# Kernel tuning notes

Hardware: AMD Instinct MI355X
Metric: run time of the kernel (lower is better)

Reference implementation:

```python
import jax, jax.numpy as jnp
import numpy as np

L, D, F, H, E, V = 16, 256, 512, 8, 12, 52000  # layers, width, FFWidth, heads, experts, vocab
B, S = 4, 512
HD = D // H
EPS = 1e-5


def _ln(x, s, b):
    m = x.mean(-1, keepdims=True)
    v = ((x - m) ** 2).mean(-1, keepdims=True)
    return (x - m) / jnp.sqrt(v + EPS) * s + b


def setup_inputs() -> dict:
    key = jax.random.key(0)
    ks = jax.random.split(key, 12)
    w = lambda k, shape: (jax.random.normal(k, shape, dtype=jnp.float32) * 0.02)
    return {
        "tokens": jax.random.randint(ks[0], (B, S), 0, V),
        "emb": w(ks[1], (V, D)),
        "Wq": w(ks[2], (L, D, D)), "bq": jnp.zeros((L, D), jnp.float32),
        "Wk": w(ks[3], (L, D, D)), "bk": jnp.zeros((L, D), jnp.float32),
        "Wv": w(ks[4], (L, D, D)), "bv": jnp.zeros((L, D), jnp.float32),
        "ln1_s": jnp.ones((L, D), jnp.float32), "ln1_b": jnp.zeros((L, D), jnp.float32),
        "ln2_s": jnp.ones((L, D), jnp.float32), "ln2_b": jnp.zeros((L, D), jnp.float32),
        "gW": w(ks[5], (L, D, E)), "gb": jnp.zeros((L, E), jnp.float32),
        "ff1W": w(ks[6], (L, E, D, F)), "ff1b": jnp.zeros((L, E, F), jnp.float32),
        "ffGW": w(ks[7], (L, E, D, F)), "ffGb": jnp.zeros((L, E, F), jnp.float32),
        "ff2W": w(ks[8], (L, E, F, D)), "ff2b": jnp.zeros((L, E, D), jnp.float32),
    }


def _forward(tokens, emb, Wq, bq, Wk, bk, Wv, bv, ln1_s, ln1_b, ln2_s, ln2_b,
             gW, gb, ff1W, ff1b, ffGW, ffGb, ff2W, ff2b):
    x = emb[tokens]  # [B,S,D]
    causal = jnp.triu(jnp.full((S, S), -jnp.inf, dtype=x.dtype), 1)

    def body(x, p):
        (wq, bq_, wk, bk_, wv, bv_, l1s, l1b, l2s, l2b,
         gw, gb_, f1w, f1b, fgw, fgb, f2w, f2b) = p
        q = (x @ wq + bq_).reshape(B, S, H, HD)
        k = (x @ wk + bk_).reshape(B, S, H, HD)
        v = (x @ wv + bv_).reshape(B, S, H, HD)
        # NOTE: original applies no 1/sqrt(d) scaling -- kept faithful
        att = jnp.einsum('bshw,bShw->bhsS', q, k) + causal
        att = jax.nn.softmax(att, axis=-1)
        o = jnp.einsum('bhsS,bShw->bshw', att, v).reshape(B, S, D)
        norm = _ln(o + x, l1s, l1b)
        # MoE: top-2 experts, outputs SUMMED (no gate weighting, per original)
        probs = jax.nn.softmax(norm @ gw + gb_, axis=-1)
        _, idx = jax.lax.top_k(probs, 2)  # [B,S,2]
        msk = jax.nn.one_hot(idx, E, dtype=norm.dtype).sum(-2)  # [B,S,E] in {0,1}
        h = jax.nn.silu(jnp.einsum('bsd,edf->bsef', norm, f1w) + f1b) \
            * (jnp.einsum('bsd,edf->bsef', norm, fgw) + fgb)
        y = jnp.einsum('bsef,efd->bsed', h, f2w) + f2b
        moe = jnp.einsum('bsed,bse->bsd', y, msk)
        return _ln(moe + norm, l2s, l2b), None

    x, _ = jax.lax.scan(body, x, (Wq, bq, Wk, bk, Wv, bv, ln1_s, ln1_b, ln2_s, ln2_b,
                                  gW, gb, ff1W, ff1b, ffGW, ffGb, ff2W, ff2b))
    return x


def reference(tokens, emb, Wq, bq, Wk, bk, Wv, bv, ln1_s, ln1_b, ln2_s, ln2_b,
              gW, gb, ff1W, ff1b, ffGW, ffGb, ff2W, ff2b):
    return _forward(tokens, emb, Wq, bq, Wk, bk, Wv, bv, ln1_s, ln1_b, ln2_s, ln2_b,
                    gW, gb, ff1W, ff1b, ffGW, ffGb, ff2W, ff2b)
```

## Files before the change

### kernel.cpp

```cpp
#include <hip/hip_runtime.h>
#include <math.h>

#define LNUM 16
#define D 256
#define FF 512
#define NH 8
#define NE 12
#define HD 32
#define BB 4
#define SS 512
#define NT 2048
#define EPS 1e-5f
#define MAXT 48
#define PADROWS 5632

typedef _Float16 f16;
typedef __attribute__((ext_vector_type(8))) _Float16 f16x8;
typedef __attribute__((ext_vector_type(4))) _Float16 f16x4;
typedef __attribute__((ext_vector_type(4))) float f32x4;
#define MFMA(A, B, C) __builtin_amdgcn_mfma_f32_16x16x32_f16((A), (B), (C), 0, 0, 0)

__device__ inline void splitf(float x, f16& h, f16& l) {
  f16 hh = (f16)x;
  h = hh;
  l = (f16)(x - (float)hh);
}

__global__ __launch_bounds__(256) void k_wprep(const float* __restrict__ src,
                                               f16* __restrict__ dh, f16* __restrict__ dl,
                                               int K, int N) {
  const size_t msz = (size_t)K * N * blockIdx.z;
  src += msz; dh += msz; dl += msz;
  const int n0 = blockIdx.x * 32, k0 = blockIdx.y * 32;
  __shared__ f16 th[32][36], tl[32][36];
  const int t = threadIdx.x;
  {
    const int r = t >> 3, c4 = (t & 7) * 4;
    float4 v = *(const float4*)(src + (size_t)(k0 + r) * N + n0 + c4);
    f16 h0, l0, h1, l1, h2, l2, h3, l3;
    splitf(v.x, h0, l0); splitf(v.y, h1, l1);
    splitf(v.z, h2, l2); splitf(v.w, h3, l3);
    th[c4 + 0][r] = h0; tl[c4 + 0][r] = l0;
    th[c4 + 1][r] = h1; tl[c4 + 1][r] = l1;
    th[c4 + 2][r] = h2; tl[c4 + 2][r] = l2;
    th[c4 + 3][r] = h3; tl[c4 + 3][r] = l3;
  }
  __syncthreads();
  const int rn = t >> 3, ck = (t & 7) * 4;
  f16x4 hv, lv;
#pragma unroll
  for (int j = 0; j < 4; j++) { hv[j] = th[rn][ck + j]; lv[j] = tl[rn][ck + j]; }
  *(f16x4*)(dh + (size_t)(n0 + rn) * K + k0 + ck) = hv;
  *(f16x4*)(dl + (size_t)(n0 + rn) * K + k0 + ck) = lv;
}

__global__ __launch_bounds__(256) void k_embed(const int* __restrict__ tok,
                                               const float* __restrict__ emb,
                                               float* __restrict__ x,
                                               f16* __restrict__ xh, f16* __restrict__ xl) {
  int n = blockIdx.x, t = threadIdx.x;
  float val = emb[(size_t)tok[n] * D + t];
  x[(size_t)n * D + t] = val;
  f16 h, l; splitf(val, h, l);
  xh[(size_t)n * D + t] = h;
  xl[(size_t)n * D + t] = l;
}

__global__ __launch_bounds__(256) void k_qkv_mfma(
    const f16* __restrict__ xh, const f16* __restrict__ xl,
    const f16* __restrict__ wqh, const f16* __restrict__ wql, const float* __restrict__ bq,
    const f16* __restrict__ wkh, const f16* __restrict__ wkl, const float* __restrict__ bk,
    const f16* __restrict__ wvh, const f16* __restrict__ wvl, const float* __restrict__ bv,
    f16* __restrict__ qhb, f16* __restrict__ qlb,
    f16* __restrict__ khb, f16* __restrict__ klb,
    f16* __restrict__ vhb, f16* __restrict__ vlb) {
  const f16* Wh; const f16* Wl; const float* bias; f16* outh; f16* outl;
  if (blockIdx.z == 0)      { Wh = wqh; Wl = wql; bias = bq; outh = qhb; outl = qlb; }
  else if (blockIdx.z == 1) { Wh = wkh; Wl = wkl; bias = bk; outh = khb; outl = klb; }
  else                      { Wh = wvh; Wl = wvl; bias = bv; outh = vhb; outl = vlb; }
  const int row0 = blockIdx.x * 128, col0 = blockIdx.y * 64;
  __shared__ f16 Ah[128][44], Al[128][44], Bh[64][44], Bl[64][44];
  const int tid = threadIdx.x;
  const int asr = tid >> 1, asc = (tid & 1) * 16;
  const int bn2 = tid >> 2, bkc = (tid & 3) * 8;
  const int lane = tid & 63, w = tid >> 6;
  const int lm = lane & 15, lg = lane >> 4, lk = lg * 8;
  f32x4 acc[2][4] = {};
  for (int k0 = 0; k0 < D; k0 += 32) {
    {
      size_t ga = (size_t)(row0 + asr) * D + k0 + asc;
      *(f16x8*)&Ah[asr][asc]     = *(const f16x8*)(xh + ga);
      *(f16x8*)&Ah[asr][asc + 8] = *(const f16x8*)(xh + ga + 8);
      *(f16x8*)&Al[asr][asc]     = *(const f16x8*)(xl + ga);
      *(f16x8*)&Al[asr][asc + 8] = *(const f16x8*)(xl + ga + 8);
      size_t gb = (size_t)(col0 + bn2) * D + k0 + bkc;
      *(f16x8*)&Bh[bn2][bkc] = *(const f16x8*)(Wh + gb);
      *(f16x8*)&Bl[bn2][bkc] = *(const f16x8*)(Wl + gb);
    }
    __syncthreads();
    f16x8 a_h[2], a_l[2];
#pragma unroll
    for (int mt = 0; mt < 2; mt++) {
      a_h[mt] = *(const f16x8*)&Ah[w * 32 + mt * 16 + lm][lk];
      a_l[mt] = *(const f16x8*)&Al[w * 32 + mt * 16 + lm][lk];
    }
#pragma unroll
    for (int nt = 0; nt < 4; nt++) {
      f16x8 b_h = *(const f16x8*)&Bh[nt * 16 + lm][lk];
      f16x8 b_l = *(const f16x8*)&Bl[nt * 16 + lm][lk];
#pragma unroll
      for (int mt = 0; mt < 2; mt++) {
        f32x4 c = acc[mt][nt];
        c = MFMA(a_h[mt], b_h, c);
        c = MFMA(a_h[mt], b_l, c);
        c = MFMA(a_l[mt], b_h, c);
        acc[mt][nt] = c;
      }
    }
    __syncthreads();
  }
#pragma unroll
  for (int mt = 0; mt < 2; mt++)
#pragma unroll
    for (int nt = 0; nt < 4; nt++) {
      int col = col0 + nt * 16 + lm;
      float bv_ = bias[col];
#pragma unroll
      for (int r = 0; r < 4; r++) {
        int row = row0 + w * 32 + mt * 16 + lg * 4 + r;
        float val = acc[mt][nt][r] + bv_;
        f16 h16, l16; splitf(val, h16, l16);
        outh[(size_t)row * D + col] = h16;
        outl[(size_t)row * D + col] = l16;
      }
    }
}

__global__ __launch_bounds__(256) void k_attn_mfma(
    const f16* __restrict__ qh, const f16* __restrict__ ql,
    const f16* __restrict__ kh, const f16* __restrict__ kl,
    const f16* __restrict__ vh, const f16* __restrict__ vl,
    float* __restrict__ o) {
  const int rt = blockIdx.x, bh = blockIdx.y;
  const int b = bh >> 3, h = bh & 7;
  const int row0 = rt * 64;
  __shared__ f16 Qh[64][40], Ql[64][40], Kh[64][40], Kl[64][40];
  __shared__ f16 Vth[32][72], Vtl[32][72];
  __shared__ f16 Ph[4][16][72], Pl[4][16][72];
  const int tid = threadIdx.x;
  const int lane = tid & 63, w = tid >> 6;
  const int lm = lane & 15, lg = lane >> 4, lk = lg * 8;
  const int sr = tid >> 2, sc = (tid & 3) * 8;
  {
    size_t gq = (size_t)(b * SS + row0 + sr) * D + h * HD + sc;
    *(f16x8*)&Qh[sr][sc] = *(const f16x8*)(qh + gq);
    *(f16x8*)&Ql[sr][sc] = *(const f16x8*)(ql + gq);
  }
  f32x4 accO[2] = {};
  float mrow[4], lsum[4];
#pragma unroll
  for (int r = 0; r < 4; r++) { mrow[r] = -1e30f; lsum[r] = 0.f; }
  for (int ct = 0; ct <= rt; ct++) {
    __syncthreads();
    {
      size_t gk = (size_t)(b * SS + ct * 64 + sr) * D + h * HD + sc;
      *(f16x8*)&Kh[sr][sc] = *(const f16x8*)(kh + gk);
      *(f16x8*)&Kl[sr][sc] = *(const f16x8*)(kl + gk);
      f16x8 hv = *(const f16x8*)(vh + gk);
      f16x8 lv = *(const f16x8*)(vl + gk);
#pragma unroll
      for (int j = 0; j < 8; j++) { Vth[sc + j][sr] = hv[j]; Vtl[sc + j][sr] = lv[j]; }
    }
    __syncthreads();
    f16x8 qfh = *(const f16x8*)&Qh[w * 16 + lm][lk];
    f16x8 qfl = *(const f16x8*)&Ql[w * 16 + lm][lk];
    f32x4 s[4];
#pragma unroll
    for (int nt = 0; nt < 4; nt++) {
      f16x8 kfh = *(const f16x8*)&Kh[nt * 16 + lm][lk];
      f16x8 kfl = *(const f16x8*)&Kl[nt * 16 + lm][lk];
      f32x4 c = {};
      c = MFMA(qfh, kfh, c);
      c = MFMA(qfh, kfl, c);
      c = MFMA(qfl, kfh, c);
      s[nt] = c;
    }
    if (ct == rt) {
#pragma unroll
      for (int nt = 0; nt < 4; nt++)
#pragma unroll
        for (int r = 0; r < 4; r++)
          if (nt * 16 + lm > w * 16 + lg * 4 + r) s[nt][r] = -1e30f;
    }
    float scal[4];
#pragma unroll
    for (int r = 0; r < 4; r++) {
      float mt2 = fmaxf(fmaxf(s[0][r], s[1][r]), fmaxf(s[2][r], s[3][r]));
      mt2 = fmaxf(mt2, __shfl_xor(mt2, 1));
      mt2 = fmaxf(mt2, __shfl_xor(mt2, 2));
      mt2 = fmaxf(mt2, __shfl_xor(mt2, 4));
      mt2 = fmaxf(mt2, __shfl_xor(mt2, 8));
      float mn = fmaxf(mrow[r], mt2);
      scal[r] = expf(mrow[r] - mn);
      mrow[r] = mn;
    }
    float rs[4] = {0.f, 0.f, 0.f, 0.f};
#pragma unroll
    for (int nt = 0; nt < 4; nt++)
#pragma unroll
      for (int r = 0; r < 4; r++) {
        float pv = expf(s[nt][r] - mrow[r]);
        rs[r] += pv;
        f16 ph16, pl16; splitf(pv, ph16, pl16);
        Ph[w][lg * 4 + r][nt * 16 + lm] = ph16;
        Pl[w][lg * 4 + r][nt * 16 + lm] = pl16;
      }
#pragma unroll
    for (int r = 0; r < 4; r++) {
      rs[r] += __shfl_xor(rs[r], 1);
      rs[r] += __shfl_xor(rs[r], 2);
      rs[r] += __shfl_xor(rs[r], 4);
      rs[r] += __shfl_xor(rs[r], 8);
      lsum[r] = lsum[r] * scal[r] + rs[r];
      accO[0][r] *= scal[r];
      accO[1][r] *= scal[r];
    }
#pragma unroll
    for (int ct2 = 0; ct2 < 2; ct2++)
#pragma unroll
      for (int ks = 0; ks < 2; ks++) {
        f16x8 pa_h = *(const f16x8*)&Ph[w][lm][ks * 32 + lk];
        f16x8 pa_l = *(const f16x8*)&Pl[w][lm][ks * 32 + lk];
        f16x8 vb_h = *(const f16x8*)&Vth[ct2 * 16 + lm][ks * 32 + lk];
        f16x8 vb_l = *(const f16x8*)&Vtl[ct2 * 16 + lm][ks * 32 + lk];
        accO[ct2] = MFMA(pa_h, vb_h, accO[ct2]);
        accO[ct2] = MFMA(pa_h, vb_l, accO[ct2]);
        accO[ct2] = MFMA(pa_l, vb_h, accO[ct2]);
      }
  }
#pragma unroll
  for (int ct2 = 0; ct2 < 2; ct2++)
#pragma unroll
    for (int r = 0; r < 4; r++) {
      int grow = row0 + w * 16 + lg * 4 + r;
      o[(size_t)(b * SS + grow) * D + h * HD + ct2 * 16 + lm] = accO[ct2][r] / lsum[r];
    }
}

__global__ __launch_bounds__(256) void k_ln1gate(
    const float* __restrict__ o, const float* __restrict__ x,
    const float* __restrict__ s1, const float* __restrict__ b1,
    const float* __restrict__ gW, const float* __restrict__ gb,
    float* __restrict__ norm, f16* __restrict__ nhb, f16* __restrict__ nlb,
    int* __restrict__ eidx) {
  const int w = threadIdx.x >> 6, lane = threadIdx.x & 63;
  const int n = blockIdx.x * 4 + w;
  float val[4], s1v = 0.f, s2v = 0.f;
#pragma unroll
  for (int j = 0; j < 4; j++) {
    int d = lane + 64 * j;
    float v = o[(size_t)n * D + d] + x[(size_t)n * D + d];
    val[j] = v; s1v += v; s2v += v * v;
  }
#pragma unroll
  for (int m = 1; m < 64; m <<= 1) {
    s1v += __shfl_xor(s1v, m);
    s2v += __shfl_xor(s2v, m);
  }
  float mean = s1v * (1.f / D);
  float var = s2v * (1.f / D) - mean * mean;
  float rstd = rsqrtf(var + EPS);
  float ge[NE];
#pragma unroll
  for (int e = 0; e < NE; e++) ge[e] = 0.f;
#pragma unroll
  for (int j = 0; j < 4; j++) {
    int d = lane + 64 * j;
    float nv = (val[j] - mean) * rstd * s1[d] + b1[d];
    norm[(size_t)n * D + d] = nv;
    f16 h16, l16; splitf(nv, h16, l16);
    nhb[(size_t)n * D + d] = h16;
    nlb[(size_t)n * D + d] = l16;
    const float* gr = gW + (size_t)d * NE;
#pragma unroll
    for (int e = 0; e < NE; e++) ge[e] += nv * gr[e];
  }
#pragma unroll
  for (int m = 1; m < 64; m <<= 1)
#pragma unroll
    for (int e = 0; e < NE; e++) ge[e] += __shfl_xor(ge[e], m);
  if (lane == 0) {
#pragma unroll
    for (int e = 0; e < NE; e++) ge[e] += gb[e];
    int i1 = 0; float v1 = ge[0];
#pragma unroll
    for (int e = 1; e < NE; e++) if (ge[e] > v1) { v1 = ge[e]; i1 = e; }
    int i2 = -1; float v2 = -3.4e38f;
#pragma unroll
    for (int e = 0; e < NE; e++) if (e != i1 && ge[e] > v2) { v2 = ge[e]; i2 = e; }
    eidx[n * 2 + 0] = i1;
    eidx[n * 2 + 1] = i2;
  }
}

__global__ __launch_bounds__(256) void k_route(const int* __restrict__ eidx,
                                               int* __restrict__ rlist, int* __restrict__ tokpos,
                                               int* __restrict__ te, int* __restrict__ tbase,
                                               int* __restrict__ tnv) {
  __shared__ int cnt[NE], cur[NE], poff[NE];
  const int t = threadIdx.x;
  if (t < NE) { cnt[t] = 0; cur[t] = 0; }
  __syncthreads();
  for (int n = t; n < NT; n += 256) {
    atomicAdd(&cnt[eidx[n * 2 + 0]], 1);
    atomicAdd(&cnt[eidx[n * 2 + 1]], 1);
  }
  __syncthreads();
  if (t == 0) {
    int off = 0, ti = 0;
    for (int e = 0; e < NE; e++) {
      poff[e] = off;
      int ntl = (cnt[e] + 127) >> 7;
      for (int tt = 0; tt < ntl; tt++) {
        te[ti] = e; tbase[ti] = off + tt * 128;
        int rem = cnt[e] - tt * 128; tnv[ti] = rem < 128 ? rem : 128;
        ti++;
      }
      off += ntl * 128;
    }
    for (; ti < MAXT; ti++) te[ti] = -1;
  }
  __syncthreads();
  for (int n = t; n < NT; n += 256) {
#pragma unroll
    for (int s2 = 0; s2 < 2; s2++) {
      int e = eidx[n * 2 + s2];
      int pos = atomicAdd(&cur[e], 1);
      int row = poff[e] + pos;
      rlist[row] = n;
      tokpos[n * 2 + s2] = row;
    }
  }
}

__global__ __launch_bounds__(256) void k_ff1_mfma(
    const f16* __restrict__ nhb, const f16* __restrict__ nlb,
    const int* __restrict__ rlist,
    const int* __restrict__ te, const int* __restrict__ tbase, const int* __restrict__ tnv,
    const f16* __restrict__ w1th, const f16* __restrict__ w1tl, const float* __restrict__ b1f,
    const f16* __restrict__ wgth, const f16* __restrict__ wgtl, const float* __restrict__ bgf,
    f16* __restrict__ hhb, f16* __restrict__ hlb) {
  const int mt0 = blockIdx.x;
  const int e = te[mt0];
  if (e < 0) return;
  const int base = tbase[mt0], nv = tnv[mt0];
  const int col0 = blockIdx.y * 64;
  const f16* W1h = w1th + (size_t)e * D * FF;
  const f16* W1l = w1tl + (size_t)e * D * FF;
  const f16* Wgh = wgth + (size_t)e * D * FF;
  const f16* Wgl = wgtl + (size_t)e * D * FF;
  __shared__ f16 Ah[128][44], Al[128][44];
  __shared__ f16 B1h[64][44], B1l[64][44], B2h[64][44], B2l[64][44];
  __shared__ int rows[128];
  const int tid = threadIdx.x;
  if (tid < 128) rows[tid] = (tid < nv) ? rlist[base + tid] : 0;
  __syncthreads();
  const int asr = tid >> 1, asc = (tid & 1) * 16;
  const int bn2 = tid >> 2, bkc = (tid & 3) * 8;
  const int lane = tid & 63, w = tid >> 6;
  const int lm = lane & 15, lg = lane >> 4, lk = lg * 8;
  f32x4 acc1[2][4] = {}, acc2[2][4] = {};
  const int arow = rows[asr];
  for (int k0 = 0; k0 < D; k0 += 32) {
    {
      size_t ga = (size_t)arow * D + k0 + asc;
      *(f16x8*)&Ah[asr][asc]     = *(const f16x8*)(nhb + ga);
      *(f16x8*)&Ah[asr][asc + 8] = *(const f16x8*)(nhb + ga + 8);
      *(f16x8*)&Al[asr][asc]     = *(const f16x8*)(nlb + ga);
      *(f16x8*)&Al[asr][asc + 8] = *(const f16x8*)(nlb + ga + 8);
      size_t gb = (size_t)(col0 + bn2) * D + k0 + bkc;
      *(f16x8*)&B1h[bn2][bkc] = *(const f16x8*)(W1h + gb);
      *(f16x8*)&B1l[bn2][bkc] = *(const f16x8*)(W1l + gb);
      *(f16x8*)&B2h[bn2][bkc] = *(const f16x8*)(Wgh + gb);
      *(f16x8*)&B2l[bn2][bkc] = *(const f16x8*)(Wgl + gb);
    }
    __syncthreads();
    f16x8 a_h[2], a_l[2];
#pragma unroll
    for (int mt = 0; mt < 2; mt++) {
      a_h[mt] = *(const f16x8*)&Ah[w * 32 + mt * 16 + lm][lk];
      a_l[mt] = *(const f16x8*)&Al[w * 32 + mt * 16 + lm][lk];
    }
#pragma unroll
    for (int nt = 0; nt < 4; nt++) {
      f16x8 b_h = *(const f16x8*)&B1h[nt * 16 + lm][lk];
      f16x8 b_l = *(const f16x8*)&B1l[nt * 16 + lm][lk];
      f16x8 c_h = *(const f16x8*)&B2h[nt * 16 + lm][lk];
      f16x8 c_l = *(const f16x8*)&B2l[nt * 16 + lm][lk];
#pragma unroll
      for (int mt = 0; mt < 2; mt++) {
        f32x4 c1 = acc1[mt][nt];
        c1 = MFMA(a_h[mt], b_h, c1);
        c1 = MFMA(a_h[mt], b_l, c1);
        c1 = MFMA(a_l[mt], b_h, c1);
        acc1[mt][nt] = c1;
        f32x4 c2 = acc2[mt][nt];
        c2 = MFMA(a_h[mt], c_h, c2);
        c2 = MFMA(a_h[mt], c_l, c2);
        c2 = MFMA(a_l[mt], c_h, c2);
        acc2[mt][nt] = c2;
      }
    }
    __syncthreads();
  }
#pragma unroll
  for (int mt = 0; mt < 2; mt++)
#pragma unroll
    for (int nt = 0; nt < 4; nt++) {
      int col = col0 + nt * 16 + lm;
      float bb1 = b1f[e * FF + col], bb2 = bgf[e * FF + col];
#pragma unroll
      for (int r = 0; r < 4; r++) {
        int rit = w * 32 + mt * 16 + lg * 4 + r;
        if (rit < nv) {
          float z1 = acc1[mt][nt][r] + bb1;
          float zg = acc2[mt][nt][r] + bb2;
          float sl = z1 / (1.f + expf(-z1));
          float hv = sl * zg;
          f16 h16, l16; splitf(hv, h16, l16);
          hhb[(size_t)(base + rit) * FF + col] = h16;
          hlb[(size_t)(base + rit) * FF + col] = l16;
        }
      }
    }
}

__global__ __launch_bounds__(256) void k_ff2_mfma(
    const f16* __restrict__ hhb, const f16* __restrict__ hlb,
    const int* __restrict__ te, const int* __restrict__ tbase, const int* __restrict__ tnv,
    const f16* __restrict__ w2th, const f16* __restrict__ w2tl, const float* __restrict__ b2f,
    float* __restrict__ ybuf) {
  const int mt0 = blockIdx.x;
  const int e = te[mt0];
  if (e < 0) return;
  const int base = tbase[mt0], nv = tnv[mt0];
  const int col0 = blockIdx.y * 64;
  const f16* W2h = w2th + (size_t)e * FF * D;
  const f16* W2l = w2tl + (size_t)e * FF * D;
  __shared__ f16 Ah[128][44], Al[128][44], Bh[64][44], Bl[64][44];
  const int tid = threadIdx.x;
  const int asr = tid >> 1, asc = (tid & 1) * 16;
  const int bn2 = tid >> 2, bkc = (tid & 3) * 8;
  const int lane = tid & 63, w = tid >> 6;
  const int lm = lane & 15, lg = lane >> 4, lk = lg * 8;
  f32x4 acc[2][4] = {};
  for (int k0 = 0; k0 < FF; k0 += 32) {
    {
      size_t ga = (size_t)(base + asr) * FF + k0 + asc;
      *(f16x8*)&Ah[asr][asc]     = *(const f16x8*)(hhb + ga);
      *(f16x8*)&Ah[asr][asc + 8] = *(const f16x8*)(hhb + ga + 8);
      *(f16x8*)&Al[asr][asc]     = *(const f16x8*)(hlb + ga);
      *(f16x8*)&Al[asr][asc + 8] = *(const f16x8*)(hlb + ga + 8);
      size_t gb = (size_t)(col0 + bn2) * FF + k0 + bkc;
      *(f16x8*)&Bh[bn2][bkc] = *(const f16x8*)(W2h + gb);
      *(f16x8*)&Bl[bn2][bkc] = *(const f16x8*)(W2l + gb);
    }
    __syncthreads();
    f16x8 a_h[2], a_l[2];
#pragma unroll
    for (int mt = 0; mt < 2; mt++) {
      a_h[mt] = *(const f16x8*)&Ah[w * 32 + mt * 16 + lm][lk];
      a_l[mt] = *(const f16x8*)&Al[w * 32 + mt * 16 + lm][lk];
    }
#pragma unroll
    for (int nt = 0; nt < 4; nt++) {
      f16x8 b_h = *(const f16x8*)&Bh[nt * 16 + lm][lk];
      f16x8 b_l = *(const f16x8*)&Bl[nt * 16 + lm][lk];
#pragma unroll
      for (int mt = 0; mt < 2; mt++) {
        f32x4 c = acc[mt][nt];
        c = MFMA(a_h[mt], b_h, c);
        c = MFMA(a_h[mt], b_l, c);
        c = MFMA(a_l[mt], b_h, c);
        acc[mt][nt] = c;
      }
    }
    __syncthreads();
  }
#pragma unroll
  for (int mt = 0; mt < 2; mt++)
#pragma unroll
    for (int nt = 0; nt < 4; nt++) {
      int col = col0 + nt * 16 + lm;
      float bb = b2f[e * D + col];
#pragma unroll
      for (int r = 0; r < 4; r++) {
        int rit = w * 32 + mt * 16 + lg * 4 + r;
        if (rit < nv) ybuf[(size_t)(base + rit) * D + col] = acc[mt][nt][r] + bb;
      }
    }
}

__global__ __launch_bounds__(256) void k_ln2(
    const float* __restrict__ ybuf, const int* __restrict__ tokpos,
    const float* __restrict__ norm, const float* __restrict__ s2, const float* __restrict__ b2,
    float* __restrict__ dst, f16* __restrict__ xh, f16* __restrict__ xl) {
  const int w = threadIdx.x >> 6, lane = threadIdx.x & 63;
  const int n = blockIdx.x * 4 + w;
  const int p0 = tokpos[n * 2 + 0], p1 = tokpos[n * 2 + 1];
  float val[4], s1v = 0.f, s2v = 0.f;
#pragma unroll
  for (int j = 0; j < 4; j++) {
    int d = lane + 64 * j;
    float v = ybuf[(size_t)p0 * D + d] + ybuf[(size_t)p1 * D + d] + norm[(size_t)n * D + d];
    val[j] = v; s1v += v; s2v += v * v;
  }
#pragma unroll
  for (int m = 1; m < 64; m <<= 1) {
    s1v += __shfl_xor(s1v, m);
    s2v += __shfl_xor(s2v, m);
  }
  float mean = s1v * (1.f / D);
  float var = s2v * (1.f / D) - mean * mean;
  float rstd = rsqrtf(var + EPS);
#pragma unroll
  for (int j = 0; j < 4; j++) {
    int d = lane + 64 * j;
    float ov = (val[j] - mean) * rstd * s2[d] + b2[d];
    dst[(size_t)n * D + d] = ov;
    f16 h16, l16; splitf(ov, h16, l16);
    xh[(size_t)n * D + d] = h16;
    xl[(size_t)n * D + d] = l16;
  }
}

extern "C" void kernel_launch(void* const* d_in, const int* in_sizes, int n_in,
                              void* d_out, int out_size, void* d_ws, size_t ws_size,
                              hipStream_t stream) {
  (void)in_sizes; (void)n_in; (void)out_size; (void)ws_size;
  const int*   tok = (const int*)d_in[0];
  const float* emb = (const float*)d_in[1];
  const float* Wq  = (const float*)d_in[2];
  const float* bq  = (const float*)d_in[3];
  const float* Wk  = (const float*)d_in[4];
  const float* bk  = (const float*)d_in[5];
  const float* Wv  = (const float*)d_in[6];
  const float* bv  = (const float*)d_in[7];
  const float* l1s = (const float*)d_in[8];
  const float* l1b = (const float*)d_in[9];
  const float* l2s = (const float*)d_in[10];
  const float* l2b = (const float*)d_in[11];
  const float* gW  = (const float*)d_in[12];
  const float* gb  = (const float*)d_in[13];
  const float* f1W = (const float*)d_in[14];
  const float* f1b = (const float*)d_in[15];
  const float* fgW = (const float*)d_in[16];
  const float* fgb = (const float*)d_in[17];
  const float* f2W = (const float*)d_in[18];
  const float* f2b = (const float*)d_in[19];
  float* out = (float*)d_out;

  char* p = (char*)d_ws;
  auto alloc = [&](size_t bytes) { char* r = p; p += (bytes + 255) & ~(size_t)255; return r; };
  float* xb = (float*)alloc((size_t)NT * D * 4);
  f16* xh = (f16*)alloc((size_t)NT * D * 2);
  f16* xl = (f16*)alloc((size_t)NT * D * 2);
  f16* qhb = (f16*)alloc((size_t)NT * D * 2);
  f16* qlb = (f16*)alloc((size_t)NT * D * 2);
  f16* khb = (f16*)alloc((size_t)NT * D * 2);
  f16* klb = (f16*)alloc((size_t)NT * D * 2);
  f16* vhb = (f16*)alloc((size_t)NT * D * 2);
  f16* vlb = (f16*)alloc((size_t)NT * D * 2);
  float* ob = (float*)alloc((size_t)NT * D * 4);
  float* nb = (float*)alloc((size_t)NT * D * 4);
  f16* nhb = (f16*)alloc((size_t)NT * D * 2);
  f16* nlb = (f16*)alloc((size_t)NT * D * 2);
  f16* hhb = (f16*)alloc((size_t)PADROWS * FF * 2);
  f16* hlb = (f16*)alloc((size_t)PADROWS * FF * 2);
  float* yb = (float*)alloc((size_t)PADROWS * D * 4);
  int* eidx   = (int*)alloc((size_t)NT * 2 * 4);
  int* rlist  = (int*)alloc((size_t)PADROWS * 4);
  int* tokpos = (int*)alloc((size_t)NT * 2 * 4);
  int* te     = (int*)alloc(MAXT * 4);
  int* tbase  = (int*)alloc(MAXT * 4);
  int* tnv    = (int*)alloc(MAXT * 4);
  size_t qkvsz = (size_t)LNUM * D * D;
  size_t ffsz  = (size_t)LNUM * NE * D * FF;
  f16* wqh = (f16*)alloc(qkvsz * 2); f16* wql = (f16*)alloc(qkvsz * 2);
  f16* wkh = (f16*)alloc(qkvsz * 2); f16* wkl = (f16*)alloc(qkvsz * 2);
  f16* wvh = (f16*)alloc(qkvsz * 2); f16* wvl = (f16*)alloc(qkvsz * 2);
  f16* w1th = (f16*)alloc(ffsz * 2); f16* w1tl = (f16*)alloc(ffsz * 2);
  f16* wgth = (f16*)alloc(ffsz * 2); f16* wgtl = (f16*)alloc(ffsz * 2);
  f16* w2th = (f16*)alloc(ffsz * 2); f16* w2tl = (f16*)alloc(ffsz * 2);

  k_wprep<<<dim3(D / 32, D / 32, LNUM), 256, 0, stream>>>(Wq, wqh, wql, D, D);
  k_wprep<<<dim3(D / 32, D / 32, LNUM), 256, 0, stream>>>(Wk, wkh, wkl, D, D);
  k_wprep<<<dim3(D / 32, D / 32, LNUM), 256, 0, stream>>>(Wv, wvh, wvl, D, D);
  k_wprep<<<dim3(FF / 32, D / 32, LNUM * NE), 256, 0, stream>>>(f1W, w1th, w1tl, D, FF);
  k_wprep<<<dim3(FF / 32, D / 32, LNUM * NE), 256, 0, stream>>>(fgW, wgth, wgtl, D, FF);
  k_wprep<<<dim3(D / 32, FF / 32, LNUM * NE), 256, 0, stream>>>(f2W, w2th, w2tl, FF, D);

  k_embed<<<NT, 256, 0, stream>>>(tok, emb, xb, xh, xl);

  for (int l = 0; l < LNUM; l++) {
    k_qkv_mfma<<<dim3(16, 4, 3), 256, 0, stream>>>(
        xh, xl,
        wqh + (size_t)l * D * D, wql + (size_t)l * D * D, bq + (size_t)l * D,
        wkh + (size_t)l * D * D, wkl + (size_t)l * D * D, bk + (size_t)l * D,
        wvh + (size_t)l * D * D, wvl + (size_t)l * D * D, bv + (size_t)l * D,
        qhb, qlb, khb, klb, vhb, vlb);
    k_attn_mfma<<<dim3(8, 32), 256, 0, stream>>>(qhb, qlb, khb, klb, vhb, vlb, ob);
    k_ln1gate<<<NT / 4, 256, 0, stream>>>(ob, xb, l1s + (size_t)l * D, l1b + (size_t)l * D,
                                          gW + (size_t)l * D * NE, gb + (size_t)l * NE,
                                          nb, nhb, nlb, eidx);
    k_route<<<1, 256, 0, stream>>>(eidx, rlist, tokpos, te, tbase, tnv);
    k_ff1_mfma<<<dim3(MAXT, 8), 256, 0, stream>>>(
        nhb, nlb, rlist, te, tbase, tnv,
        w1th + (size_t)l * NE * D * FF, w1tl + (size_t)l * NE * D * FF, f1b + (size_t)l * NE * FF,
        wgth + (size_t)l * NE * D * FF, wgtl + (size_t)l * NE * D * FF, fgb + (size_t)l * NE * FF,
        hhb, hlb);
    k_ff2_mfma<<<dim3(MAXT, 4), 256, 0, stream>>>(
        hhb, hlb, te, tbase, tnv,
        w2th + (size_t)l * NE * FF * D, w2tl + (size_t)l * NE * FF * D, f2b + (size_t)l * NE * D,
        yb);
    k_ln2<<<NT / 4, 256, 0, stream>>>(yb, tokpos, nb, l2s + (size_t)l * D, l2b + (size_t)l * D,
                                      (l == LNUM - 1) ? out : xb, xh, xl);
  }
}
```

Before: 1.974 ms.

## Load MFMA operands directly from global memory, dropping LDS staging in GEMMs

The QKV, FF1 and FF2 GEMM kernels now load their A and B MFMA fragments straight from global memory into registers. This removes the shared-memory tiles and the per-iteration barriers, relying on cache hits for the operand reuse across waves. The attention kernel also keeps Q and K fragments in registers and prefetches the next V tile into registers, still transposing V and P through LDS. The trade-off is more global/L2 traffic per MFMA, since each wave re-reads the same B tiles, in exchange for fewer syncs and less LDS pressure.

```diff
diff --git a/kernel.cpp b/kernel.cpp
--- a/kernel.cpp
+++ b/kernel.cpp
@@ -74,40 +74,32 @@
     f16* __restrict__ qhb, f16* __restrict__ qlb,
     f16* __restrict__ khb, f16* __restrict__ klb,
     f16* __restrict__ vhb, f16* __restrict__ vlb) {
+  const int mat = blockIdx.y >> 2;
   const f16* Wh; const f16* Wl; const float* bias; f16* outh; f16* outl;
-  if (blockIdx.z == 0)      { Wh = wqh; Wl = wql; bias = bq; outh = qhb; outl = qlb; }
-  else if (blockIdx.z == 1) { Wh = wkh; Wl = wkl; bias = bk; outh = khb; outl = klb; }
-  else                      { Wh = wvh; Wl = wvl; bias = bv; outh = vhb; outl = vlb; }
-  const int row0 = blockIdx.x * 128, col0 = blockIdx.y * 64;
-  __shared__ f16 Ah[128][44], Al[128][44], Bh[64][44], Bl[64][44];
+  if (mat == 0)      { Wh = wqh; Wl = wql; bias = bq; outh = qhb; outl = qlb; }
+  else if (mat == 1) { Wh = wkh; Wl = wkl; bias = bk; outh = khb; outl = klb; }
+  else               { Wh = wvh; Wl = wvl; bias = bv; outh = vhb; outl = vlb; }
+  const int row0 = blockIdx.x * 128, col0 = (blockIdx.y & 3) * 64;
   const int tid = threadIdx.x;
-  const int asr = tid >> 1, asc = (tid & 1) * 16;
-  const int bn2 = tid >> 2, bkc = (tid & 3) * 8;
   const int lane = tid & 63, w = tid >> 6;
   const int lm = lane & 15, lg = lane >> 4, lk = lg * 8;
   f32x4 acc[2][4] = {};
+  const f16* arow0h = xh + (size_t)(row0 + w * 32 + lm) * D + lk;
+  const f16* arow0l = xl + (size_t)(row0 + w * 32 + lm) * D + lk;
+  const f16* bcolh = Wh + (size_t)(col0 + lm) * D + lk;
+  const f16* bcoll = Wl + (size_t)(col0 + lm) * D + lk;
+#pragma unroll 2
   for (int k0 = 0; k0 < D; k0 += 32) {
-    {
-      size_t ga = (size_t)(row0 + asr) * D + k0 + asc;
-      *(f16x8*)&Ah[asr][asc]     = *(const f16x8*)(xh + ga);
-      *(f16x8*)&Ah[asr][asc + 8] = *(const f16x8*)(xh + ga + 8);
-      *(f16x8*)&Al[asr][asc]     = *(const f16x8*)(xl + ga);
-      *(f16x8*)&Al[asr][asc + 8] = *(const f16x8*)(xl + ga + 8);
-      size_t gb = (size_t)(col0 + bn2) * D + k0 + bkc;
-      *(f16x8*)&Bh[bn2][bkc] = *(const f16x8*)(Wh + gb);
-      *(f16x8*)&Bl[bn2][bkc] = *(const f16x8*)(Wl + gb);
-    }
-    __syncthreads();
     f16x8 a_h[2], a_l[2];
 #pragma unroll
     for (int mt = 0; mt < 2; mt++) {
-      a_h[mt] = *(const f16x8*)&Ah[w * 32 + mt * 16 + lm][lk];
-      a_l[mt] = *(const f16x8*)&Al[w * 32 + mt * 16 + lm][lk];
-    }
-#pragma unroll
-    for (int nt = 0; nt < 4; nt++) {
-      f16x8 b_h = *(const f16x8*)&Bh[nt * 16 + lm][lk];
-      f16x8 b_l = *(const f16x8*)&Bl[nt * 16 + lm][lk];
+      a_h[mt] = *(const f16x8*)(arow0h + (size_t)mt * 16 * D + k0);
+      a_l[mt] = *(const f16x8*)(arow0l + (size_t)mt * 16 * D + k0);
+    }
+#pragma unroll
+    for (int nt = 0; nt < 4; nt++) {
+      f16x8 b_h = *(const f16x8*)(bcolh + (size_t)nt * 16 * D + k0);
+      f16x8 b_l = *(const f16x8*)(bcoll + (size_t)nt * 16 * D + k0);
 #pragma unroll
       for (int mt = 0; mt < 2; mt++) {
         f32x4 c = acc[mt][nt];
@@ -117,7 +109,6 @@
         acc[mt][nt] = c;
       }
     }
-    __syncthreads();
   }
 #pragma unroll
   for (int mt = 0; mt < 2; mt++)
@@ -144,41 +135,29 @@
   const int rt = blockIdx.x, bh = blockIdx.y;
   const int b = bh >> 3, h = bh & 7;
   const int row0 = rt * 64;
-  __shared__ f16 Qh[64][40], Ql[64][40], Kh[64][40], Kl[64][40];
   __shared__ f16 Vth[32][72], Vtl[32][72];
   __shared__ f16 Ph[4][16][72], Pl[4][16][72];
   const int tid = threadIdx.x;
   const int lane = tid & 63, w = tid >> 6;
   const int lm = lane & 15, lg = lane >> 4, lk = lg * 8;
   const int sr = tid >> 2, sc = (tid & 3) * 8;
-  {
-    size_t gq = (size_t)(b * SS + row0 + sr) * D + h * HD + sc;
-    *(f16x8*)&Qh[sr][sc] = *(const f16x8*)(qh + gq);
-    *(f16x8*)&Ql[sr][sc] = *(const f16x8*)(ql + gq);
-  }
+  const size_t gq = (size_t)(b * SS + row0 + w * 16 + lm) * D + h * HD + lk;
+  const f16x8 qfh = *(const f16x8*)(qh + gq);
+  const f16x8 qfl = *(const f16x8*)(ql + gq);
+  f16x8 vrh = *(const f16x8*)(vh + (size_t)(b * SS + sr) * D + h * HD + sc);
+  f16x8 vrl = *(const f16x8*)(vl + (size_t)(b * SS + sr) * D + h * HD + sc);
   f32x4 accO[2] = {};
   float mrow[4], lsum[4];
 #pragma unroll
   for (int r = 0; r < 4; r++) { mrow[r] = -1e30f; lsum[r] = 0.f; }
   for (int ct = 0; ct <= rt; ct++) {
-    __syncthreads();
-    {
-      size_t gk = (size_t)(b * SS + ct * 64 + sr) * D + h * HD + sc;
-      *(f16x8*)&Kh[sr][sc] = *(const f16x8*)(kh + gk);
-      *(f16x8*)&Kl[sr][sc] = *(const f16x8*)(kl + gk);
-      f16x8 hv = *(const f16x8*)(vh + gk);
-      f16x8 lv = *(const f16x8*)(vl + gk);
-#pragma unroll
-      for (int j = 0; j < 8; j++) { Vth[sc + j][sr] = hv[j]; Vtl[sc + j][sr] = lv[j]; }
-    }
-    __syncthreads();
-    f16x8 qfh = *(const f16x8*)&Qh[w * 16 + lm][lk];
-    f16x8 qfl = *(const f16x8*)&Ql[w * 16 + lm][lk];
     f32x4 s[4];
-#pragma unroll
-    for (int nt = 0; nt < 4; nt++) {
-      f16x8 kfh = *(const f16x8*)&Kh[nt * 16 + lm][lk];
-      f16x8 kfl = *(const f16x8*)&Kl[nt * 16 + lm][lk];
+    const f16* kbase_h = kh + (size_t)(b * SS + ct * 64 + lm) * D + h * HD + lk;
+    const f16* kbase_l = kl + (size_t)(b * SS + ct * 64 + lm) * D + h * HD + lk;
+#pragma unroll
+    for (int nt = 0; nt < 4; nt++) {
+      f16x8 kfh = *(const f16x8*)(kbase_h + (size_t)nt * 16 * D);
+      f16x8 kfl = *(const f16x8*)(kbase_l + (size_t)nt * 16 * D);
       f32x4 c = {};
       c = MFMA(qfh, kfh, c);
       c = MFMA(qfh, kfl, c);
@@ -191,6 +170,15 @@
 #pragma unroll
         for (int r = 0; r < 4; r++)
           if (nt * 16 + lm > w * 16 + lg * 4 + r) s[nt][r] = -1e30f;
+    }
+    __syncthreads();
+    {
+#pragma unroll
+      for (int j = 0; j < 8; j++) { Vth[sc + j][sr] = vrh[j]; Vtl[sc + j][sr] = vrl[j]; }
+    }
+    if (ct < rt) {
+      vrh = *(const f16x8*)(vh + (size_t)(b * SS + (ct + 1) * 64 + sr) * D + h * HD + sc);
+      vrl = *(const f16x8*)(vl + (size_t)(b * SS + (ct + 1) * 64 + sr) * D + h * HD + sc);
     }
     float scal[4];
 #pragma unroll
@@ -225,6 +213,7 @@
       accO[0][r] *= scal[r];
       accO[1][r] *= scal[r];
     }
+    __syncthreads();
 #pragma unroll
     for (int ct2 = 0; ct2 < 2; ct2++)
 #pragma unroll
@@ -355,48 +344,35 @@
   if (e < 0) return;
   const int base = tbase[mt0], nv = tnv[mt0];
   const int col0 = blockIdx.y * 64;
-  const f16* W1h = w1th + (size_t)e * D * FF;
-  const f16* W1l = w1tl + (size_t)e * D * FF;
-  const f16* Wgh = wgth + (size_t)e * D * FF;
-  const f16* Wgl = wgtl + (size_t)e * D * FF;
-  __shared__ f16 Ah[128][44], Al[128][44];
-  __shared__ f16 B1h[64][44], B1l[64][44], B2h[64][44], B2l[64][44];
-  __shared__ int rows[128];
+  const f16* W1h = w1th + (size_t)e * D * FF + (size_t)(col0) * D;
+  const f16* W1l = w1tl + (size_t)e * D * FF + (size_t)(col0) * D;
+  const f16* Wgh = wgth + (size_t)e * D * FF + (size_t)(col0) * D;
+  const f16* Wgl = wgtl + (size_t)e * D * FF + (size_t)(col0) * D;
   const int tid = threadIdx.x;
-  if (tid < 128) rows[tid] = (tid < nv) ? rlist[base + tid] : 0;
-  __syncthreads();
-  const int asr = tid >> 1, asc = (tid & 1) * 16;
-  const int bn2 = tid >> 2, bkc = (tid & 3) * 8;
   const int lane = tid & 63, w = tid >> 6;
   const int lm = lane & 15, lg = lane >> 4, lk = lg * 8;
+  int ra[2];
+#pragma unroll
+  for (int mt = 0; mt < 2; mt++) {
+    int slot = w * 32 + mt * 16 + lm;
+    ra[mt] = (slot < nv) ? rlist[base + slot] : 0;
+  }
   f32x4 acc1[2][4] = {}, acc2[2][4] = {};
-  const int arow = rows[asr];
+#pragma unroll 2
   for (int k0 = 0; k0 < D; k0 += 32) {
-    {
-      size_t ga = (size_t)arow * D + k0 + asc;
-      *(f16x8*)&Ah[asr][asc]     = *(const f16x8*)(nhb + ga);
-      *(f16x8*)&Ah[asr][asc + 8] = *(const f16x8*)(nhb + ga + 8);
-      *(f16x8*)&Al[asr][asc]     = *(const f16x8*)(nlb + ga);
-      *(f16x8*)&Al[asr][asc + 8] = *(const f16x8*)(nlb + ga + 8);
-      size_t gb = (size_t)(col0 + bn2) * D + k0 + bkc;
-      *(f16x8*)&B1h[bn2][bkc] = *(const f16x8*)(W1h + gb);
-      *(f16x8*)&B1l[bn2][bkc] = *(const f16x8*)(W1l + gb);
-      *(f16x8*)&B2h[bn2][bkc] = *(const f16x8*)(Wgh + gb);
-      *(f16x8*)&B2l[bn2][bkc] = *(const f16x8*)(Wgl + gb);
-    }
-    __syncthreads();
     f16x8 a_h[2], a_l[2];
 #pragma unroll
     for (int mt = 0; mt < 2; mt++) {
-      a_h[mt] = *(const f16x8*)&Ah[w * 32 + mt * 16 + lm][lk];
-      a_l[mt] = *(const f16x8*)&Al[w * 32 + mt * 16 + lm][lk];
-    }
-#pragma unroll
-    for (int nt = 0; nt < 4; nt++) {
-      f16x8 b_h = *(const f16x8*)&B1h[nt * 16 + lm][lk];
-      f16x8 b_l = *(const f16x8*)&B1l[nt * 16 + lm][lk];
-      f16x8 c_h = *(const f16x8*)&B2h[nt * 16 + lm][lk];
-      f16x8 c_l = *(const f16x8*)&B2l[nt * 16 + lm][lk];
+      a_h[mt] = *(const f16x8*)(nhb + (size_t)ra[mt] * D + k0 + lk);
+      a_l[mt] = *(const f16x8*)(nlb + (size_t)ra[mt] * D + k0 + lk);
+    }
+#pragma unroll
+    for (int nt = 0; nt < 4; nt++) {
+      size_t gb = (size_t)(nt * 16 + lm) * D + k0 + lk;
+      f16x8 b_h = *(const f16x8*)(W1h + gb);
+      f16x8 b_l = *(const f16x8*)(W1l + gb);
+      f16x8 c_h = *(const f16x8*)(Wgh + gb);
+      f16x8 c_l = *(const f16x8*)(Wgl + gb);
 #pragma unroll
       for (int mt = 0; mt < 2; mt++) {
         f32x4 c1 = acc1[mt][nt];
@@ -411,7 +387,6 @@
         acc2[mt][nt] = c2;
       }
     }
-    __syncthreads();
   }
 #pragma unroll
   for (int mt = 0; mt < 2; mt++)
@@ -445,37 +420,27 @@
   if (e < 0) return;
   const int base = tbase[mt0], nv = tnv[mt0];
   const int col0 = blockIdx.y * 64;
-  const f16* W2h = w2th + (size_t)e * FF * D;
-  const f16* W2l = w2tl + (size_t)e * FF * D;
-  __shared__ f16 Ah[128][44], Al[128][44], Bh[64][44], Bl[64][44];
+  const f16* W2h = w2th + (size_t)e * FF * D + (size_t)col0 * FF;
+  const f16* W2l = w2tl + (size_t)e * FF * D + (size_t)col0 * FF;
   const int tid = threadIdx.x;
-  const int asr = tid >> 1, asc = (tid & 1) * 16;
-  const int bn2 = tid >> 2, bkc = (tid & 3) * 8;
   const int lane = tid & 63, w = tid >> 6;
   const int lm = lane & 15, lg = lane >> 4, lk = lg * 8;
+  const f16* arowh = hhb + (size_t)(base + w * 32 + lm) * FF + lk;
+  const f16* arowl = hlb + (size_t)(base + w * 32 + lm) * FF + lk;
   f32x4 acc[2][4] = {};
+#pragma unroll 2
   for (int k0 = 0; k0 < FF; k0 += 32) {
-    {
-      size_t ga = (size_t)(base + asr) * FF + k0 + asc;
-      *(f16x8*)&Ah[asr][asc]     = *(const f16x8*)(hhb + ga);
-      *(f16x8*)&Ah[asr][asc + 8] = *(const f16x8*)(hhb + ga + 8);
-      *(f16x8*)&Al[asr][asc]     = *(const f16x8*)(hlb + ga);
-      *(f16x8*)&Al[asr][asc + 8] = *(const f16x8*)(hlb + ga + 8);
-      size_t gb = (size_t)(col0 + bn2) * FF + k0 + bkc;
-      *(f16x8*)&Bh[bn2][bkc] = *(const f16x8*)(W2h + gb);
-      *(f16x8*)&Bl[bn2][bkc] = *(const f16x8*)(W2l + gb);
-    }
-    __syncthreads();
     f16x8 a_h[2], a_l[2];
 #pragma unroll
     for (int mt = 0; mt < 2; mt++) {
-      a_h[mt] = *(const f16x8*)&Ah[w * 32 + mt * 16 + lm][lk];
-      a_l[mt] = *(const f16x8*)&Al[w * 32 + mt * 16 + lm][lk];
-    }
-#pragma unroll
-    for (int nt = 0; nt < 4; nt++) {
-      f16x8 b_h = *(const f16x8*)&Bh[nt * 16 + lm][lk];
-      f16x8 b_l = *(const f16x8*)&Bl[nt * 16 + lm][lk];
+      a_h[mt] = *(const f16x8*)(arowh + (size_t)mt * 16 * FF + k0);
+      a_l[mt] = *(const f16x8*)(arowl + (size_t)mt * 16 * FF + k0);
+    }
+#pragma unroll
+    for (int nt = 0; nt < 4; nt++) {
+      size_t gb = (size_t)(nt * 16 + lm) * FF + k0 + lk;
+      f16x8 b_h = *(const f16x8*)(W2h + gb);
+      f16x8 b_l = *(const f16x8*)(W2l + gb);
 #pragma unroll
       for (int mt = 0; mt < 2; mt++) {
         f32x4 c = acc[mt][nt];
@@ -485,7 +450,6 @@
         acc[mt][nt] = c;
       }
     }
-    __syncthreads();
   }
 #pragma unroll
   for (int mt = 0; mt < 2; mt++)
@@ -603,7 +567,7 @@
   k_embed<<<NT, 256, 0, stream>>>(tok, emb, xb, xh, xl);
 
   for (int l = 0; l < LNUM; l++) {
-    k_qkv_mfma<<<dim3(16, 4, 3), 256, 0, stream>>>(
+    k_qkv_mfma<<<dim3(16, 12), 256, 0, stream>>>(
         xh, xl,
         wqh + (size_t)l * D * D, wql + (size_t)l * D * D, bq + (size_t)l * D,
         wkh + (size_t)l * D * D, wkl + (size_t)l * D * D, bk + (size_t)l * D,
```

Result: slower. 2.504 ms (+26.9%).
